# Kernel optimization log

Hardware: AMD Instinct MI355X
Metric: run time of the kernel (lower is better)

The kernel has to match this reference:

```python
import math
import jax, jax.numpy as jnp
import numpy as np

B, S, D, H = 2, 2048, 1024, 16
HD = D // H
I = 3752  # round(1024 * 11/3 / 8) * 8, per GluMLP default
EPS = 1e-6


def _alibi_bias(nheads, n):
    # AlibiPostionEmbedding: slopes (power-of-2 formula) * -1, times |i-j|
    start = 2.0 ** (-(2.0 ** (-(math.log2(nheads) - 3))))
    slopes = np.array([start * start ** i for i in range(nheads)], dtype=np.float64) * -1.0
    pos = np.arange(n)
    rel = np.abs(pos[None, :] - pos[:, None])  # [n, n]
    return jnp.asarray(slopes[:, None, None] * rel[None, :, :], dtype=jnp.float32)


def rmsnorm(h, w):
    h32 = h.astype(jnp.float32)
    var = jnp.mean(h32 * h32, axis=-1, keepdims=True)
    return (w * (h32 * jax.lax.rsqrt(var + EPS))).astype(h.dtype)


def setup_inputs() -> dict:
    key = jax.random.key(0)
    ks = jax.random.split(key, 16)
    sd = 1.0 / math.sqrt(D)
    si = 1.0 / math.sqrt(I)
    rn = lambda k, shape, s: jax.random.normal(k, shape, jnp.float32) * s
    return {
        "x": rn(ks[0], (B, S, D), 1.0),
        "wq": rn(ks[1], (D, D), sd), "bq": rn(ks[2], (D,), 0.02),
        "wk": rn(ks[3], (D, D), sd), "bk": rn(ks[4], (D,), 0.02),
        "wv": rn(ks[5], (D, D), sd), "bv": rn(ks[6], (D,), 0.02),
        "wo": rn(ks[7], (D, D), sd), "bo": rn(ks[8], (D,), 0.02),
        "w_gate": rn(ks[9], (D, I), sd),
        "w_up": rn(ks[10], (D, I), sd),
        "w_down": rn(ks[11], (I, D), si),
        "ln1_w": jnp.ones((D,), jnp.float32),
        "ln2_w": jnp.ones((D,), jnp.float32),
        "attn_bias": _alibi_bias(H, S),                       # [H, S, S]
        "tgt_mask": jnp.triu(jnp.ones((S, S), bool), 1),      # causal, True = masked
        "key_padding_mask": jnp.zeros((B, S), bool),          # True = padded
    }


def reference(x, wq, bq, wk, bk, wv, bv, wo, bo, w_gate, w_up, w_down,
              ln1_w, ln2_w, attn_bias, tgt_mask, key_padding_mask):
    # ---- TransformerEncoderLayer.forward (eval mode: dropout = identity) ----
    residual = x
    h = rmsnorm(x, ln1_w)
    # MultiheadAttention with ALiBi bias + fused bool masks
    q = (h @ wq + bq).reshape(B, S, H, HD)
    k = (h @ wk + bk).reshape(B, S, H, HD)
    v = (h @ wv + bv).reshape(B, S, H, HD)
    scores = jnp.einsum("bqhd,bkhd->bhqk", q, k) * (HD ** -0.5)  # [B,H,S,S]
    scores = scores + attn_bias[None]
    mask = tgt_mask[None, :, :] | key_padding_mask[:, None, :]   # [B,S,S]
    scores = jnp.where(mask[:, None, :, :], -jnp.inf, scores)
    probs = jax.nn.softmax(scores, axis=-1)
    attn = jnp.einsum("bhqk,bkhd->bqhd", probs, v).reshape(B, S, D)
    attn = attn @ wo + bo
    residual = attn + residual
    # GluMLP (SwiGLU)
    h2 = rmsnorm(residual, ln2_w)
    mlp = (jax.nn.silu(h2 @ w_gate) * (h2 @ w_up)) @ w_down
    return mlp + residual
```

## Files before the change

### kernel.cpp

```cpp
#include <hip/hip_runtime.h>
#include <hip/hip_bf16.h>
#include <cmath>

typedef __bf16 bf16_t;
typedef __bf16 bf16x8 __attribute__((ext_vector_type(8)));
typedef short  s16x8  __attribute__((ext_vector_type(8)));
typedef float  f32x4  __attribute__((ext_vector_type(4)));

static constexpr int Bn  = 2;
static constexpr int Sn  = 2048;
static constexpr int Dn  = 1024;
static constexpr int Hn  = 16;
static constexpr int In  = 3752;
static constexpr int Mn  = Bn * Sn;
static constexpr int Ipad = 3840;

__device__ __forceinline__ void cp16(const bf16_t* g, bf16_t* l) {
  __builtin_amdgcn_global_load_lds(
      (const __attribute__((address_space(1))) unsigned int*)g,
      (__attribute__((address_space(3))) unsigned int*)l, 16, 0, 0);
}

struct TransJob  { const float* src; bf16_t* dst; int R, C; };
struct TransJobs { TransJob j[7]; };

__global__ __launch_bounds__(256) void k_transpose_all(TransJobs jobs) {
  const TransJob jb = jobs.j[blockIdx.z];
  const int c0 = blockIdx.x * 32, r0 = blockIdx.y * 32;
  if (c0 >= jb.C || r0 >= jb.R) return;
  __shared__ float tile[32][33];
  const int tx = threadIdx.x & 31, ty = threadIdx.x >> 5;
#pragma unroll
  for (int e = 0; e < 4; ++e) {
    int r = r0 + ty + e * 8, c = c0 + tx;
    if (r < jb.R && c < jb.C) tile[ty + e * 8][tx] = jb.src[(size_t)r * jb.C + c];
  }
  __syncthreads();
#pragma unroll
  for (int e = 0; e < 4; ++e) {
    int c = c0 + ty + e * 8, r = r0 + tx;
    if (r < jb.R && c < jb.C) jb.dst[(size_t)c * jb.R + r] = (bf16_t)tile[tx][ty + e * 8];
  }
}

__global__ __launch_bounds__(256) void k_rmsnorm(const float* __restrict__ in,
                                                 const float* __restrict__ w,
                                                 bf16_t* __restrict__ out) {
  const int row = blockIdx.x;
  const int tid = threadIdx.x;
  const float* ip = in + (size_t)row * Dn;
  float v[4];
  float ss = 0.f;
#pragma unroll
  for (int e = 0; e < 4; ++e) {
    v[e] = ip[tid + e * 256];
    ss += v[e] * v[e];
  }
  for (int off = 32; off > 0; off >>= 1) ss += __shfl_down(ss, off);
  __shared__ float red[4];
  if ((tid & 63) == 0) red[tid >> 6] = ss;
  __syncthreads();
  float tot = red[0] + red[1] + red[2] + red[3];
  float sc = rsqrtf(tot * (1.0f / Dn) + 1e-6f);
  bf16_t* op = out + (size_t)row * Dn;
#pragma unroll
  for (int e = 0; e < 4; ++e) {
    int idx = tid + e * 256;
    op[idx] = (bf16_t)(w[idx] * v[e] * sc);
  }
}

__global__ __launch_bounds__(256) void k_gemm64(
    const bf16_t* __restrict__ A, const bf16_t* __restrict__ Bt,
    const float* __restrict__ bias, const float* __restrict__ resid,
    float* __restrict__ outf, int N, int K, int lda, int ldb) {
  __shared__ bf16_t As[64 * 64];
  __shared__ bf16_t Bs[128 * 64];
  const int m0 = blockIdx.x * 64, n0 = blockIdx.y * 128;
  const int tid = threadIdx.x;
  const int lane = tid & 63, wid = tid >> 6;
  const int wc = wid * 32;
  const int l15 = lane & 15, quad = lane >> 4;
  const int sw = l15 & 7;
  const int srow_lo = lane >> 3, pchunk = lane & 7;

  f32x4 acc[4][2];
  const f32x4 z4 = {0.f, 0.f, 0.f, 0.f};
#pragma unroll
  for (int i = 0; i < 4; ++i)
#pragma unroll
    for (int j = 0; j < 2; ++j) acc[i][j] = z4;

  for (int k0 = 0; k0 < K; k0 += 64) {
#pragma unroll
    for (int c = 0; c < 2; ++c) {
      const int r = (wid * 2 + c) * 8 + srow_lo;
      const int gc = pchunk ^ (r & 7);
      cp16(A + (size_t)(m0 + r) * lda + k0 + gc * 8, As + (wid * 2 + c) * 512);
    }
#pragma unroll
    for (int c = 0; c < 4; ++c) {
      const int r = (wid * 4 + c) * 8 + srow_lo;
      const int gc = pchunk ^ (r & 7);
      cp16(Bt + (size_t)(n0 + r) * ldb + k0 + gc * 8, Bs + (wid * 4 + c) * 512);
    }
    __syncthreads();
#pragma unroll
    for (int kh = 0; kh < 2; ++kh) {
      const int ph = ((kh * 4 + quad) ^ sw) * 8;
      bf16x8 af[4], bfr[2];
#pragma unroll
      for (int i = 0; i < 4; ++i)
        af[i] = *(const bf16x8*)(As + (i * 16 + l15) * 64 + ph);
#pragma unroll
      for (int j = 0; j < 2; ++j)
        bfr[j] = *(const bf16x8*)(Bs + (wc + j * 16 + l15) * 64 + ph);
#pragma unroll
      for (int i = 0; i < 4; ++i)
#pragma unroll
        for (int j = 0; j < 2; ++j)
          acc[i][j] = __builtin_amdgcn_mfma_f32_16x16x32_bf16(af[i], bfr[j], acc[i][j], 0, 0, 0);
    }
    __syncthreads();
  }

#pragma unroll
  for (int i = 0; i < 4; ++i)
#pragma unroll
    for (int j = 0; j < 2; ++j) {
      const int col = n0 + wc + j * 16 + l15;
      const float bval = bias ? bias[col] : 0.f;
#pragma unroll
      for (int r = 0; r < 4; ++r) {
        const int row = m0 + i * 16 + quad * 4 + r;
        const size_t idx = (size_t)row * N + col;
        outf[idx] = acc[i][j][r] + bval + (resid ? resid[idx] : 0.f);
      }
    }
}

__global__ __launch_bounds__(256) void k_gemm_qkv(
    const bf16_t* __restrict__ A, const bf16_t* __restrict__ Bt,
    const float* __restrict__ bq, const float* __restrict__ bk,
    const float* __restrict__ bv, bf16_t* __restrict__ qkvb) {
  __shared__ bf16_t As[128 * 64];
  __shared__ bf16_t Bs[128 * 64];
  const int m0 = blockIdx.x * 128, n0 = blockIdx.y * 128;
  const int tid = threadIdx.x;
  const int lane = tid & 63, wid = tid >> 6;
  const int wr = (wid >> 1) * 64, wc = (wid & 1) * 64;
  const int l15 = lane & 15, quad = lane >> 4;
  const int sw = l15 & 7;
  const int srow_lo = lane >> 3, pchunk = lane & 7;

  f32x4 acc[4][4];
  const f32x4 z4 = {0.f, 0.f, 0.f, 0.f};
#pragma unroll
  for (int i = 0; i < 4; ++i)
#pragma unroll
    for (int j = 0; j < 4; ++j) acc[i][j] = z4;

  for (int k0 = 0; k0 < Dn; k0 += 64) {
#pragma unroll
    for (int c = 0; c < 4; ++c) {
      const int r = (wid * 4 + c) * 8 + srow_lo;
      const int gc = pchunk ^ (r & 7);
      cp16(A  + (size_t)(m0 + r) * Dn + k0 + gc * 8, As + (wid * 4 + c) * 512);
      cp16(Bt + (size_t)(n0 + r) * Dn + k0 + gc * 8, Bs + (wid * 4 + c) * 512);
    }
    __syncthreads();
#pragma unroll
    for (int kh = 0; kh < 2; ++kh) {
      bf16x8 af[4], bfr[4];
      const int ph = ((kh * 4 + quad) ^ sw) * 8;
#pragma unroll
      for (int i = 0; i < 4; ++i)
        af[i] = *(const bf16x8*)(As + (wr + i * 16 + l15) * 64 + ph);
#pragma unroll
      for (int j = 0; j < 4; ++j)
        bfr[j] = *(const bf16x8*)(Bs + (wc + j * 16 + l15) * 64 + ph);
#pragma unroll
      for (int i = 0; i < 4; ++i)
#pragma unroll
        for (int j = 0; j < 4; ++j)
          acc[i][j] = __builtin_amdgcn_mfma_f32_16x16x32_bf16(af[i], bfr[j], acc[i][j], 0, 0, 0);
    }
    __syncthreads();
  }

#pragma unroll
  for (int i = 0; i < 4; ++i)
#pragma unroll
    for (int j = 0; j < 4; ++j) {
      const int col = n0 + wc + j * 16 + l15;
      const int sel = col >> 10;
      const float bval = (sel == 0) ? bq[col] : (sel == 1) ? bk[col - 1024] : bv[col - 2048];
#pragma unroll
      for (int r = 0; r < 4; ++r) {
        const int row = m0 + wr + i * 16 + quad * 4 + r;
        qkvb[(size_t)row * 3072 + col] = (bf16_t)(acc[i][j][r] + bval);
      }
    }
}

__global__ __launch_bounds__(256) void k_gemm_gateup(
    const bf16_t* __restrict__ A, const bf16_t* __restrict__ Bg,
    const bf16_t* __restrict__ Bu, bf16_t* __restrict__ out, int N, int ldo) {
  __shared__ bf16_t As[128 * 64];
  __shared__ bf16_t Gs[128 * 64];
  __shared__ bf16_t Us[128 * 64];
  const int m0 = blockIdx.x * 128, n0 = blockIdx.y * 128;
  const int tid = threadIdx.x;
  const int lane = tid & 63, wid = tid >> 6;
  const int wr = (wid >> 1) * 64, wc = (wid & 1) * 64;
  const int l15 = lane & 15, quad = lane >> 4;
  const int sw = l15 & 7;
  const int srow_lo = lane >> 3, pchunk = lane & 7;

  f32x4 accg[4][4], accu[4][4];
  const f32x4 z4 = {0.f, 0.f, 0.f, 0.f};
#pragma unroll
  for (int i = 0; i < 4; ++i)
#pragma unroll
    for (int j = 0; j < 4; ++j) { accg[i][j] = z4; accu[i][j] = z4; }

  for (int k0 = 0; k0 < Dn; k0 += 64) {
#pragma unroll
    for (int c = 0; c < 4; ++c) {
      const int r = (wid * 4 + c) * 8 + srow_lo;
      const int gc = pchunk ^ (r & 7);
      const int nb = min(n0 + r, N - 1);
      cp16(A  + (size_t)(m0 + r) * Dn + k0 + gc * 8, As + (wid * 4 + c) * 512);
      cp16(Bg + (size_t)nb * Dn + k0 + gc * 8, Gs + (wid * 4 + c) * 512);
      cp16(Bu + (size_t)nb * Dn + k0 + gc * 8, Us + (wid * 4 + c) * 512);
    }
    __syncthreads();
#pragma unroll
    for (int kh = 0; kh < 2; ++kh) {
      bf16x8 af[4], gf[4], uf[4];
      const int ph = ((kh * 4 + quad) ^ sw) * 8;
#pragma unroll
      for (int i = 0; i < 4; ++i)
        af[i] = *(const bf16x8*)(As + (wr + i * 16 + l15) * 64 + ph);
#pragma unroll
      for (int j = 0; j < 4; ++j) {
        gf[j] = *(const bf16x8*)(Gs + (wc + j * 16 + l15) * 64 + ph);
        uf[j] = *(const bf16x8*)(Us + (wc + j * 16 + l15) * 64 + ph);
      }
#pragma unroll
      for (int i = 0; i < 4; ++i)
#pragma unroll
        for (int j = 0; j < 4; ++j) {
          accg[i][j] = __builtin_amdgcn_mfma_f32_16x16x32_bf16(af[i], gf[j], accg[i][j], 0, 0, 0);
          accu[i][j] = __builtin_amdgcn_mfma_f32_16x16x32_bf16(af[i], uf[j], accu[i][j], 0, 0, 0);
        }
    }
    __syncthreads();
  }

#pragma unroll
  for (int i = 0; i < 4; ++i)
#pragma unroll
    for (int j = 0; j < 4; ++j) {
      const int col = n0 + wc + j * 16 + l15;
#pragma unroll
      for (int r = 0; r < 4; ++r) {
        const int row = m0 + wr + i * 16 + quad * 4 + r;
        const float g = accg[i][j][r];
        const float u = accu[i][j][r];
        const float sl = g / (1.f + expf(-g));
        out[(size_t)row * ldo + col] = (col < N) ? (bf16_t)(sl * u) : (bf16_t)0.f;
      }
    }
}

__global__ __launch_bounds__(256) void k_attn(
    const bf16_t* __restrict__ qkv, bf16_t* __restrict__ Ob) {
  const int qt = (int)gridDim.x - 1 - (int)blockIdx.x;
  const int h  = blockIdx.y;
  const int b  = blockIdx.z;
  constexpr int LDK = 72, LDP = 76;
  __shared__ bf16_t Ks[64 * LDK];
  __shared__ bf16_t Vt[64 * LDK];
  __shared__ bf16_t Ps[4][32 * LDP];

  const int tid  = threadIdx.x;
  const int lane = tid & 63, w = tid >> 6;
  const int l15  = lane & 15, quad = lane >> 4;

  constexpr float L2E = 1.4426950408889634f;
  const float slopeL = -exp2f(-0.5f * (float)(h + 1)) * L2E;

  bf16x8 aq[2][2];
#pragma unroll
  for (int g = 0; g < 2; ++g) {
    const int row = qt * 128 + w * 32 + g * 16 + l15;
    const bf16_t* qp = qkv + (size_t)(b * Sn + row) * 3072 + h * 64;
    aq[g][0] = *(const bf16x8*)(qp + quad * 8);
    aq[g][1] = *(const bf16x8*)(qp + 32 + quad * 8);
#pragma unroll
    for (int e = 0; e < 8; ++e) {
      aq[g][0][e] = (bf16_t)((float)aq[g][0][e] * 0.125f);
      aq[g][1][e] = (bf16_t)((float)aq[g][1][e] * 0.125f);
    }
  }

  int qrow[2];
  float rowterm[2][4];
#pragma unroll
  for (int g = 0; g < 2; ++g) {
    qrow[g] = qt * 128 + w * 32 + g * 16 + quad * 4;
#pragma unroll
    for (int rr = 0; rr < 4; ++rr) rowterm[g][rr] = slopeL * (float)(qrow[g] + rr);
  }
  float colbase[4];
#pragma unroll
  for (int t = 0; t < 4; ++t) colbase[t] = slopeL * (float)(t * 16 + l15);

  f32x4 o[2][4], lacc[2];
  const f32x4 z4 = {0.f, 0.f, 0.f, 0.f};
#pragma unroll
  for (int g = 0; g < 2; ++g) {
    lacc[g] = z4;
#pragma unroll
    for (int dt = 0; dt < 4; ++dt) o[g][dt] = z4;
  }
  bf16x8 ones;
#pragma unroll
  for (int e = 0; e < 8; ++e) ones[e] = (bf16_t)1.0f;

  const int r = tid >> 2, c0e = (tid & 3) * 16;
  const size_t kbase = (size_t)(b * Sn + r) * 3072 + 1024 + h * 64 + c0e;
  const size_t step  = (size_t)64 * 3072;

  s16x8 kr0 = *(const s16x8*)(qkv + kbase);
  s16x8 kr1 = *(const s16x8*)(qkv + kbase + 8);
  s16x8 vr0 = *(const s16x8*)(qkv + kbase + 1024);
  s16x8 vr1 = *(const s16x8*)(qkv + kbase + 1024 + 8);

  const int nkt = 2 * qt + 2;
  for (int kt = 0; kt < nkt; ++kt) {
    __syncthreads();
    *(s16x8*)(Ks + r * LDK + c0e)     = kr0;
    *(s16x8*)(Ks + r * LDK + c0e + 8) = kr1;
    {
      const bf16x8 v0 = *(const bf16x8*)&vr0, v1 = *(const bf16x8*)&vr1;
#pragma unroll
      for (int e = 0; e < 8; ++e) {
        Vt[(c0e + e) * LDK + r]     = v0[e];
        Vt[(c0e + 8 + e) * LDK + r] = v1[e];
      }
    }
    __syncthreads();
    if (kt + 1 < nkt) {
      const size_t kb = kbase + (size_t)(kt + 1) * step;
      kr0 = *(const s16x8*)(qkv + kb);
      kr1 = *(const s16x8*)(qkv + kb + 8);
      vr0 = *(const s16x8*)(qkv + kb + 1024);
      vr1 = *(const s16x8*)(qkv + kb + 1024 + 8);
    }

    const float kofs = slopeL * (float)(kt * 64);
    const bool diag = (kt + 2 >= nkt);

#pragma unroll
    for (int g = 0; g < 2; ++g) {
      f32x4 s[4];
#pragma unroll
      for (int t = 0; t < 4; ++t) s[t] = z4;
#pragma unroll
      for (int t = 0; t < 4; ++t) {
        bf16x8 bk0 = *(const bf16x8*)(Ks + (t * 16 + l15) * LDK + quad * 8);
        bf16x8 bk1 = *(const bf16x8*)(Ks + (t * 16 + l15) * LDK + 32 + quad * 8);
        s[t] = __builtin_amdgcn_mfma_f32_16x16x32_bf16(aq[g][0], bk0, s[t], 0, 0, 0);
        s[t] = __builtin_amdgcn_mfma_f32_16x16x32_bf16(aq[g][1], bk1, s[t], 0, 0, 0);
      }
#pragma unroll
      for (int t = 0; t < 4; ++t) {
        const int j = kt * 64 + t * 16 + l15;
#pragma unroll
        for (int rr = 0; rr < 4; ++rr) {
          float v2 = fmaf(s[t][rr], L2E, rowterm[g][rr] - (kofs + colbase[t]));
          if (diag && j > qrow[g] + rr) v2 = -3.0e38f;
          Ps[w][(g * 16 + quad * 4 + rr) * LDP + t * 16 + l15] = (bf16_t)exp2f(v2);
        }
      }
    }

#pragma unroll
    for (int g = 0; g < 2; ++g) {
#pragma unroll
      for (int kh = 0; kh < 2; ++kh) {
        bf16x8 pa = *(const bf16x8*)(Ps[w] + (g * 16 + l15) * LDP + kh * 32 + quad * 8);
        lacc[g] = __builtin_amdgcn_mfma_f32_16x16x32_bf16(pa, ones, lacc[g], 0, 0, 0);
#pragma unroll
        for (int dt = 0; dt < 4; ++dt) {
          bf16x8 bv = *(const bf16x8*)(Vt + (dt * 16 + l15) * LDK + kh * 32 + quad * 8);
          o[g][dt] = __builtin_amdgcn_mfma_f32_16x16x32_bf16(pa, bv, o[g][dt], 0, 0, 0);
        }
      }
    }
  }

#pragma unroll
  for (int g = 0; g < 2; ++g)
#pragma unroll
    for (int rr = 0; rr < 4; ++rr) {
      const float inv = 1.f / lacc[g][rr];
      bf16_t* op = Ob + (size_t)(b * Sn + qrow[g] + rr) * 1024 + h * 64;
#pragma unroll
      for (int dt = 0; dt < 4; ++dt)
        op[dt * 16 + l15] = (bf16_t)(o[g][dt][rr] * inv);
    }
}

extern "C" void kernel_launch(void* const* d_in, const int* in_sizes, int n_in,
                              void* d_out, int out_size, void* d_ws, size_t ws_size,
                              hipStream_t stream) {
  (void)in_sizes; (void)n_in; (void)out_size; (void)ws_size;
  const float* x   = (const float*)d_in[0];
  const float* wq  = (const float*)d_in[1];
  const float* bq  = (const float*)d_in[2];
  const float* wk_ = (const float*)d_in[3];
  const float* bk  = (const float*)d_in[4];
  const float* wv  = (const float*)d_in[5];
  const float* bv  = (const float*)d_in[6];
  const float* wo  = (const float*)d_in[7];
  const float* bo  = (const float*)d_in[8];
  const float* wg  = (const float*)d_in[9];
  const float* wu  = (const float*)d_in[10];
  const float* wd  = (const float*)d_in[11];
  const float* ln1 = (const float*)d_in[12];
  const float* ln2 = (const float*)d_in[13];

  char* base = (char*)d_ws;
  const size_t MiB = 1024 * 1024;
  bf16_t* h1    = (bf16_t*)(base);
  bf16_t* wqkvT = (bf16_t*)(base + 8  * MiB);
  bf16_t* woT   = (bf16_t*)(base + 16 * MiB);
  bf16_t* wgT   = (bf16_t*)(base + 24 * MiB);
  bf16_t* wuT   = (bf16_t*)(base + 32 * MiB);
  bf16_t* wdT   = (bf16_t*)(base + 40 * MiB);
  bf16_t* qkvb  = (bf16_t*)(base + 48 * MiB);
  float*  res1  = (float*) (base + 72 * MiB);
  bf16_t* mlp   = (bf16_t*)(base + 88 * MiB);
  bf16_t* attnb = (bf16_t*)d_out;
  bf16_t* h2    = (bf16_t*)d_out;

  const dim3 blk(256);

  TransJobs jobs;
  jobs.j[0] = {wq,  wqkvT,                      Dn, Dn};
  jobs.j[1] = {wk_, wqkvT + (size_t)Dn * Dn,    Dn, Dn};
  jobs.j[2] = {wv,  wqkvT + 2 * (size_t)Dn * Dn, Dn, Dn};
  jobs.j[3] = {wo,  woT, Dn, Dn};
  jobs.j[4] = {wg,  wgT, Dn, In};
  jobs.j[5] = {wu,  wuT, Dn, In};
  jobs.j[6] = {wd,  wdT, In, Dn};
  k_transpose_all<<<dim3(118, 118, 7), blk, 0, stream>>>(jobs);

  k_rmsnorm<<<dim3(Mn), blk, 0, stream>>>(x, ln1, h1);

  k_gemm_qkv<<<dim3(Mn / 128, 3072 / 128), blk, 0, stream>>>(h1, wqkvT, bq, bk, bv, qkvb);

  k_attn<<<dim3(Sn / 128, Hn, Bn), blk, 0, stream>>>(qkvb, attnb);

  k_gemm64<<<dim3(Mn / 64, Dn / 128), blk, 0, stream>>>(
      attnb, woT, bo, x, res1, Dn, Dn, Dn, Dn);

  k_rmsnorm<<<dim3(Mn), blk, 0, stream>>>(res1, ln2, h2);

  k_gemm_gateup<<<dim3(Mn / 128, Ipad / 128), blk, 0, stream>>>(
      h2, wgT, wuT, mlp, In, Ipad);

  k_gemm64<<<dim3(Mn / 64, Dn / 128), blk, 0, stream>>>(
      mlp, wdT, nullptr, res1, (float*)d_out, Dn, Ipad, Ipad, In);
}
```

Measured before the change: 739.3 us.

## Remap GEMM blocks for XCD-aware L2 locality and compact transpose grid

Each GEMM now launches on a 1D grid. A mapping function first assigns contiguous tile ranges to each of the 8 XCDs (workgroups are dispatched round-robin across XCDs), then groups tiles into bands of 8 M-rows so that blocks sharing A and B tiles run on the same XCD's L2. The weight transpose kernel moves from a padded 118x118x7 grid, which mostly early-exits, to a compact 1D grid with per-job start offsets. The aim is better L2 hit rates and fewer wasted block launches. The mapping assumes the tile count divides by 8 and M-blocks by 8, which holds for these shapes.

```diff
diff --git a/kernel.cpp b/kernel.cpp
--- a/kernel.cpp
+++ b/kernel.cpp
@@ -21,13 +21,28 @@
       (__attribute__((address_space(3))) unsigned int*)l, 16, 0, 0);
 }
 
-struct TransJob  { const float* src; bf16_t* dst; int R, C; };
+__device__ __forceinline__ void xcd_map(int bid, int nM, int nN, int& m, int& n) {
+  const int q = (nM * nN) >> 3;
+  const int L = (bid & 7) * q + (bid >> 3);
+  const int bandw = nN << 3;
+  const int band = L / bandw;
+  const int rem  = L - band * bandw;
+  n = rem >> 3;
+  m = (band << 3) + (rem & 7);
+}
+
+struct TransJob  { const float* src; bf16_t* dst; int R, C, bx, start; };
 struct TransJobs { TransJob j[7]; };
 
 __global__ __launch_bounds__(256) void k_transpose_all(TransJobs jobs) {
-  const TransJob jb = jobs.j[blockIdx.z];
-  const int c0 = blockIdx.x * 32, r0 = blockIdx.y * 32;
-  if (c0 >= jb.C || r0 >= jb.R) return;
+  const int bid = blockIdx.x;
+  int jj = 0;
+#pragma unroll
+  for (int t = 1; t < 7; ++t)
+    if (bid >= jobs.j[t].start) jj = t;
+  const TransJob jb = jobs.j[jj];
+  const int local = bid - jb.start;
+  const int r0 = (local / jb.bx) * 32, c0 = (local % jb.bx) * 32;
   __shared__ float tile[32][33];
   const int tx = threadIdx.x & 31, ty = threadIdx.x >> 5;
 #pragma unroll
@@ -73,10 +88,12 @@
 __global__ __launch_bounds__(256) void k_gemm64(
     const bf16_t* __restrict__ A, const bf16_t* __restrict__ Bt,
     const float* __restrict__ bias, const float* __restrict__ resid,
-    float* __restrict__ outf, int N, int K, int lda, int ldb) {
+    float* __restrict__ outf, int N, int K, int lda, int ldb, int nN) {
   __shared__ bf16_t As[64 * 64];
   __shared__ bf16_t Bs[128 * 64];
-  const int m0 = blockIdx.x * 64, n0 = blockIdx.y * 128;
+  int mblk, nblk;
+  xcd_map(blockIdx.x, Mn / 64, nN, mblk, nblk);
+  const int m0 = mblk * 64, n0 = nblk * 128;
   const int tid = threadIdx.x;
   const int lane = tid & 63, wid = tid >> 6;
   const int wc = wid * 32;
@@ -145,7 +162,9 @@
     const float* __restrict__ bv, bf16_t* __restrict__ qkvb) {
   __shared__ bf16_t As[128 * 64];
   __shared__ bf16_t Bs[128 * 64];
-  const int m0 = blockIdx.x * 128, n0 = blockIdx.y * 128;
+  int mblk, nblk;
+  xcd_map(blockIdx.x, Mn / 128, 3072 / 128, mblk, nblk);
+  const int m0 = mblk * 128, n0 = nblk * 128;
   const int tid = threadIdx.x;
   const int lane = tid & 63, wid = tid >> 6;
   const int wr = (wid >> 1) * 64, wc = (wid & 1) * 64;
@@ -209,7 +228,9 @@
   __shared__ bf16_t As[128 * 64];
   __shared__ bf16_t Gs[128 * 64];
   __shared__ bf16_t Us[128 * 64];
-  const int m0 = blockIdx.x * 128, n0 = blockIdx.y * 128;
+  int mblk, nblk;
+  xcd_map(blockIdx.x, Mn / 128, Ipad / 128, mblk, nblk);
+  const int m0 = mblk * 128, n0 = nblk * 128;
   const int tid = threadIdx.x;
   const int lane = tid & 63, wid = tid >> 6;
   const int wr = (wid >> 1) * 64, wc = (wid & 1) * 64;
@@ -450,29 +471,36 @@
   const dim3 blk(256);
 
   TransJobs jobs;
-  jobs.j[0] = {wq,  wqkvT,                      Dn, Dn};
-  jobs.j[1] = {wk_, wqkvT + (size_t)Dn * Dn,    Dn, Dn};
-  jobs.j[2] = {wv,  wqkvT + 2 * (size_t)Dn * Dn, Dn, Dn};
-  jobs.j[3] = {wo,  woT, Dn, Dn};
-  jobs.j[4] = {wg,  wgT, Dn, In};
-  jobs.j[5] = {wu,  wuT, Dn, In};
-  jobs.j[6] = {wd,  wdT, In, Dn};
-  k_transpose_all<<<dim3(118, 118, 7), blk, 0, stream>>>(jobs);
+  int start = 0;
+  auto setjob = [&](int idx, const float* s, bf16_t* d, int R, int C) {
+    const int bx = (C + 31) / 32, by = (R + 31) / 32;
+    jobs.j[idx] = {s, d, R, C, bx, start};
+    start += bx * by;
+  };
+  setjob(0, wq,  wqkvT,                       Dn, Dn);
+  setjob(1, wk_, wqkvT + (size_t)Dn * Dn,     Dn, Dn);
+  setjob(2, wv,  wqkvT + 2 * (size_t)Dn * Dn, Dn, Dn);
+  setjob(3, wo,  woT, Dn, Dn);
+  setjob(4, wg,  wgT, Dn, In);
+  setjob(5, wu,  wuT, Dn, In);
+  setjob(6, wd,  wdT, In, Dn);
+  k_transpose_all<<<dim3(start), blk, 0, stream>>>(jobs);
 
   k_rmsnorm<<<dim3(Mn), blk, 0, stream>>>(x, ln1, h1);
 
-  k_gemm_qkv<<<dim3(Mn / 128, 3072 / 128), blk, 0, stream>>>(h1, wqkvT, bq, bk, bv, qkvb);
+  k_gemm_qkv<<<dim3((Mn / 128) * (3072 / 128)), blk, 0, stream>>>(
+      h1, wqkvT, bq, bk, bv, qkvb);
 
   k_attn<<<dim3(Sn / 128, Hn, Bn), blk, 0, stream>>>(qkvb, attnb);
 
-  k_gemm64<<<dim3(Mn / 64, Dn / 128), blk, 0, stream>>>(
-      attnb, woT, bo, x, res1, Dn, Dn, Dn, Dn);
+  k_gemm64<<<dim3((Mn / 64) * (Dn / 128)), blk, 0, stream>>>(
+      attnb, woT, bo, x, res1, Dn, Dn, Dn, Dn, Dn / 128);
 
   k_rmsnorm<<<dim3(Mn), blk, 0, stream>>>(res1, ln2, h2);
 
-  k_gemm_gateup<<<dim3(Mn / 128, Ipad / 128), blk, 0, stream>>>(
+  k_gemm_gateup<<<dim3((Mn / 128) * (Ipad / 128)), blk, 0, stream>>>(
       h2, wgT, wuT, mlp, In, Ipad);
 
-  k_gemm64<<<dim3(Mn / 64, Dn / 128), blk, 0, stream>>>(
-      mlp, wdT, nullptr, res1, (float*)d_out, Dn, Ipad, Ipad, In);
-}
+  k_gemm64<<<dim3((Mn / 64) * (Dn / 128)), blk, 0, stream>>>(
+      mlp, wdT, nullptr, res1, (float*)d_out, Dn, Ipad, Ipad, In, Dn / 128);
+}
```

Measured after the change: 731.8 us. No clear change (-1.0%).
